# Optimization experiments

Hardware: AMD Instinct MI355X
Metric: run time of the kernel (lower is better)

The kernel has to match this reference:

```python
import jax, jax.numpy as jnp
import numpy as np

B, T, F_, H = 128, 256, 36, 128
FREQ_INV = jnp.array([1.0 / 24.0, 1.0 / 168.0, 1.0 / 720.0], dtype=jnp.float32)
WRT = 0.1


def setup_inputs() -> dict:
    key = jax.random.key(0)
    ks = jax.random.split(key, 20)

    def unif(k, shape, s):
        return jax.random.uniform(k, shape, jnp.float32, -s, s)

    sH = 1.0 / np.sqrt(H)
    sF = 1.0 / np.sqrt(F_)
    s2F = 1.0 / np.sqrt(2 * F_)

    # data layout: [B, 24, T, F]; forward direction uses channels 0..11:
    # 0 originals, 1 masks (binary), 2 deltas (nonneg), 3/6/9 remainders,
    # 4/7/10 trends, 5/8/11 seasonals.
    data = jax.random.normal(ks[0], (B, 24, T, F_), dtype=jnp.float32)
    masks = (jax.random.uniform(ks[1], (B, T, F_)) > 0.2).astype(jnp.float32)
    deltas = jax.random.uniform(ks[2], (B, T, F_)) * 5.0
    data = data.at[:, 1, :, :].set(masks)
    data = data.at[:, 2, :, :].set(deltas)

    return {
        "data": data,
        "W_dh": unif(ks[3], (H, F_), sH),   # TemporalDecay(F->H)
        "b_dh": unif(ks[4], (H,), sH),
        "W_dx": unif(ks[5], (F_, F_), sF),  # TemporalDecay diag (F->F)
        "b_dx": unif(ks[6], (F_,), sF),
        "W_hist": unif(ks[7], (F_, H), sH),  # Linear(H, F)
        "b_hist": unif(ks[8], (F_,), sH),
        "W_feat": unif(ks[9], (F_, F_), sF),
        "b_feat": unif(ks[10], (F_,), sF),
        "W_wc": unif(ks[11], (F_, 2 * F_), s2F),  # Linear(2F, F)
        "b_wc": unif(ks[12], (F_,), s2F),
        "W_ih": unif(ks[13], (4 * H, 2 * F_), sH),  # LSTMCell
        "W_hh": unif(ks[14], (4 * H, H), sH),
        "b_ih": unif(ks[15], (4 * H,), sH),
        "b_hh": unif(ks[16], (4 * H,), sH),
        "W_comb": jax.random.normal(ks[17], (1, 3), dtype=jnp.float32),  # weight_sumone_linear(3,1)
    }


def reference(data, W_dh, b_dh, W_dx, b_dx, W_hist, b_hist, W_feat, b_feat,
              W_wc, b_wc, W_ih, W_hh, b_ih, b_hh, W_comb):
    Bn, _, Tn, Fd = data.shape
    Hh = W_hh.shape[1]

    masks = data[:, 1]   # [B,T,F]
    deltas = data[:, 2]
    r = jnp.stack([data[:, 3], data[:, 6], data[:, 9]], axis=1)    # [B,3,T,F]
    tr = jnp.stack([data[:, 4], data[:, 7], data[:, 10]], axis=1)
    se = jnp.stack([data[:, 5], data[:, 8], data[:, 11]], axis=1)

    # time-major for scan
    m_T = jnp.moveaxis(masks, 1, 0)    # [T,B,F]
    d_T = jnp.moveaxis(deltas, 1, 0)
    r_T = jnp.moveaxis(r, 2, 0)        # [T,B,3,F]
    tr_T = jnp.moveaxis(tr, 2, 0)
    se_T = jnp.moveaxis(se, 2, 0)

    wk = jax.nn.softmax(W_comb, axis=1)[0]          # [3], sums to 1
    Wf_masked = W_feat * (1.0 - jnp.eye(Fd, dtype=data.dtype))
    w_dx_diag = jnp.diagonal(W_dx)                   # diag TemporalDecay
    reg_term = WRT * jnp.sum(wk * FREQ_INV)          # added every timestep

    def comb(x):  # weight_sumone_linear over the 3-decomposition axis
        return jnp.einsum('bkf,k->bf', x, wk)

    def step(carry, xs):
        h, c, loss = carry
        m2, d2, rt, trt, st = xs
        m = jnp.broadcast_to(m2[:, None, :], rt.shape)  # [B,3,F]
        d = jnp.broadcast_to(d2[:, None, :], rt.shape)

        gamma_h = jnp.exp(-jax.nn.relu(jnp.einsum('bkf,hf->bkh', d, W_dh) + b_dh))
        gamma_x = jnp.exp(-jax.nn.relu(d * w_dx_diag + b_dx))
        h = h * gamma_h

        x_h = jnp.einsum('bkh,fh->bkf', h, W_hist) + b_hist
        denom = jnp.sum(comb(m)) + 1e-5
        loss = loss + jnp.sum(comb(jnp.abs(rt - x_h) * m)) / denom

        x_c = m * rt + (1.0 - m) * x_h
        z_h = jnp.einsum('bkf,gf->bkg', x_c, Wf_masked) + b_feat
        loss = loss + jnp.sum(comb(jnp.abs(rt - z_h) * m)) / denom

        alpha = jnp.einsum('bkf,gf->bkg', jnp.concatenate([gamma_x, m], axis=2), W_wc) + b_wc
        c_h = alpha * z_h + (1.0 - alpha) * x_h
        loss = loss + jnp.sum(comb(jnp.abs(rt - c_h) * m)) / denom
        loss = loss + reg_term

        c_c = m * rt + (1.0 - m) * c_h
        inp = jnp.concatenate([c_c, m], axis=2).reshape(-1, 2 * Fd)  # [B*3, 2F]
        hf = h.reshape(-1, Hh)
        cf = c.reshape(-1, Hh)
        # PyTorch LSTMCell: gates ordered i, f, g, o. (dropout is identity in eval)
        gates = inp @ W_ih.T + b_ih + hf @ W_hh.T + b_hh
        i, f, g, o = jnp.split(gates, 4, axis=1)
        cf = jax.nn.sigmoid(f) * cf + jax.nn.sigmoid(i) * jnp.tanh(g)
        hf = jax.nn.sigmoid(o) * jnp.tanh(cf)
        h = hf.reshape(-1, 3, Hh)
        c = cf.reshape(-1, 3, Hh)

        impute = comb(c_c + st + trt)  # [B,F]
        return (h, c, loss), impute

    h0 = jnp.zeros((Bn, 3, Hh), dtype=data.dtype)
    c0 = jnp.zeros((Bn, 3, Hh), dtype=data.dtype)
    (hT, cT, loss), imput_T = jax.lax.scan(
        step, (h0, c0, jnp.float32(0.0)), (m_T, d_T, r_T, tr_T, se_T))
    imputations = jnp.moveaxis(imput_T, 0, 1)  # [B,T,F]
    return loss, imputations
```

## Files before the change

kernel.cpp:

```cpp
#include <hip/hip_runtime.h>
#include <math.h>

#define Bn 128
#define Tn 256
#define Fn 36
#define Hn 128
#define G4 512
#define BTFn (Bn*Tn*Fn)
#define TF 9216

#define INVD_OFF 0
#define LOSS_OFF 102656
#define IMP_OFF  103040

#define OFF_WHIST  0
#define OFF_WF     2304
#define OFF_WWC    2952
#define OFF_WDHT   4248
#define OFF_IN     6552
#define OFF_DP     6732
#define OFF_MP     6752
#define OFF_GXP    6792
#define OFF_XCP    6812
#define OFF_CCP    6832
#define OFF_ALPHA  6852
#define OFF_HP     6888
#define OFF_GF     6952
#define OFF_INVD   7464
#define OFF_BH     7720
#define OFF_BF     7756
#define OFF_BWC    7792
#define OFF_BDH    7828
#define OFF_WDXD   7956
#define OFF_BDX    7992
#define SMEM_WORDS 8028

typedef _Float16 h2_t __attribute__((ext_vector_type(2)));

__device__ __forceinline__ unsigned int bcu(float x) { return __builtin_bit_cast(unsigned int, x); }
__device__ __forceinline__ unsigned int pkh(float a, float b) {
    return __builtin_bit_cast(unsigned int, __builtin_amdgcn_cvt_pkrtz(a, b));
}
__device__ __forceinline__ float dot2(unsigned int a, unsigned int b, float c) {
    return __builtin_amdgcn_fdot2(__builtin_bit_cast(h2_t, a), __builtin_bit_cast(h2_t, b), c, false);
}
__device__ __forceinline__ float sigmoid_f(float x) {
    return __builtin_amdgcn_rcpf(1.f + __expf(-x));
}
__device__ __forceinline__ float tanh_f(float x) {
    return fmaf(2.f, __builtin_amdgcn_rcpf(1.f + __expf(-2.f * x)), -1.f);
}

__global__ void prep_kernel(const float* __restrict__ data,
                            float* __restrict__ ws) {
    int t = blockIdx.x;
    int tid = threadIdx.x;
    __shared__ float red[256];
    float s = 0.f;
    for (int idx = tid; idx < Bn * Fn; idx += 256) {
        int b = idx / Fn, f = idx - b * Fn;
        s += data[((size_t)(b * 24 + 1) * Tn + t) * Fn + f];
    }
    red[tid] = s;
    __syncthreads();
    for (int off = 128; off > 0; off >>= 1) {
        if (tid < off) red[tid] += red[tid + off];
        __syncthreads();
    }
    if (tid == 0) ws[INVD_OFF + t] = 1.f / (red[0] + 1e-5f);
}

#define DOT18(acc, base, woff) do {                                    \
    const unsigned int* _p = &smem[(base)];                            \
    float _a = 0.f, _b = 0.f;                                          \
    float4 _v0 = *(const float4*)_p;                                   \
    _a = dot2(bcu(_v0.x), wi[(woff) + 0], _a);                         \
    _b = dot2(bcu(_v0.y), wi[(woff) + 1], _b);                         \
    _a = dot2(bcu(_v0.z), wi[(woff) + 2], _a);                         \
    _b = dot2(bcu(_v0.w), wi[(woff) + 3], _b);                         \
    float4 _v1 = *(const float4*)(_p + 4);                             \
    _a = dot2(bcu(_v1.x), wi[(woff) + 4], _a);                         \
    _b = dot2(bcu(_v1.y), wi[(woff) + 5], _b);                         \
    _a = dot2(bcu(_v1.z), wi[(woff) + 6], _a);                         \
    _b = dot2(bcu(_v1.w), wi[(woff) + 7], _b);                         \
    float4 _v2 = *(const float4*)(_p + 8);                             \
    _a = dot2(bcu(_v2.x), wi[(woff) + 8], _a);                         \
    _b = dot2(bcu(_v2.y), wi[(woff) + 9], _b);                         \
    _a = dot2(bcu(_v2.z), wi[(woff) + 10], _a);                        \
    _b = dot2(bcu(_v2.w), wi[(woff) + 11], _b);                        \
    float4 _v3 = *(const float4*)(_p + 12);                            \
    _a = dot2(bcu(_v3.x), wi[(woff) + 12], _a);                        \
    _b = dot2(bcu(_v3.y), wi[(woff) + 13], _b);                        \
    _a = dot2(bcu(_v3.z), wi[(woff) + 14], _a);                        \
    _b = dot2(bcu(_v3.w), wi[(woff) + 15], _b);                        \
    float2 _v4 = *(const float2*)(_p + 16);                            \
    _a = dot2(bcu(_v4.x), wi[(woff) + 16], _a);                        \
    _b = dot2(bcu(_v4.y), wi[(woff) + 17], _b);                        \
    acc += _a + _b;                                                    \
} while (0)

#define STAGE(v, P) do {                                                          \
    if (lw == 0) {                                                                \
        *(float4*)&smf[OFF_IN + 4 * lu] = (v);                                    \
        smem[OFF_MP + (P) * 20 + 2 * lu]     = pkh((v).x, (v).y);                 \
        smem[OFF_MP + (P) * 20 + 2 * lu + 1] = pkh((v).z, (v).w);                 \
    } else if (lw == 1) {                                                         \
        smem[OFF_DP + 2 * lu]     = pkh((v).x, (v).y);                            \
        smem[OFF_DP + 2 * lu + 1] = pkh((v).z, (v).w);                            \
        float4 _wd = *(const float4*)&smf[OFF_WDXD + 4 * lu];                     \
        float4 _bd = *(const float4*)&smf[OFF_BDX + 4 * lu];                      \
        float _g0 = __expf(-fmaxf(fmaf((v).x, _wd.x, _bd.x), 0.f));               \
        float _g1 = __expf(-fmaxf(fmaf((v).y, _wd.y, _bd.y), 0.f));               \
        float _g2 = __expf(-fmaxf(fmaf((v).z, _wd.z, _bd.z), 0.f));               \
        float _g3 = __expf(-fmaxf(fmaf((v).w, _wd.w, _bd.w), 0.f));               \
        smem[OFF_GXP + 2 * lu]     = pkh(_g0, _g1);                               \
        smem[OFF_GXP + 2 * lu + 1] = pkh(_g2, _g3);                               \
    } else {                                                                      \
        *(float4*)&smf[OFF_IN + lw * 36 + 4 * lu] = (v);                          \
    }                                                                             \
} while (0)

__global__ __launch_bounds__(512) void rits_main(
    const float* __restrict__ data,
    const float* __restrict__ W_dh, const float* __restrict__ b_dh,
    const float* __restrict__ W_dx, const float* __restrict__ b_dx,
    const float* __restrict__ W_hist, const float* __restrict__ b_hist,
    const float* __restrict__ W_feat, const float* __restrict__ b_feat,
    const float* __restrict__ W_wc, const float* __restrict__ b_wc,
    const float* __restrict__ W_ih, const float* __restrict__ W_hh,
    const float* __restrict__ b_ih, const float* __restrict__ b_hh,
    const float* __restrict__ W_comb,
    float* __restrict__ ws) {

    extern __shared__ unsigned int smem[];
    float* smf = (float*)smem;

    const int tid = threadIdx.x;
    const int chain = blockIdx.x;
    const int b = chain / 3, k = chain - 3 * b;

    for (int i = tid; i < 64 * Fn; i += 512) {
        int q = i / Fn, f = i - q * Fn;
        float2 wv = *(const float2*)&W_hist[f * Hn + 2 * q];
        smem[OFF_WHIST + i] = pkh(wv.x, wv.y);
    }
    for (int i = tid; i < 18 * Fn; i += 512) {
        int q = i / Fn, g = i - q * Fn;
        float2 wv = *(const float2*)&W_feat[g * Fn + 2 * q];
        float w0 = (2 * q     == g) ? 0.f : wv.x;
        float w1 = (2 * q + 1 == g) ? 0.f : wv.y;
        smem[OFF_WF + i] = pkh(w0, w1);
    }
    for (int i = tid; i < 36 * Fn; i += 512) {
        int q = i / Fn, g = i - q * Fn;
        int col = (q < 18) ? 2 * q : Fn + 2 * (q - 18);
        float2 wv = *(const float2*)&W_wc[g * 2 * Fn + col];
        smem[OFF_WWC + i] = pkh(wv.x, wv.y);
    }
    for (int i = tid; i < 18 * 128; i += 512) {
        int q = i >> 7, u = i & 127;
        float2 wv = *(const float2*)&W_dh[u * Fn + 2 * q];
        smem[OFF_WDHT + i] = pkh(wv.x, wv.y);
    }
    if (tid < Fn) {
        smf[OFF_BH + tid]   = b_hist[tid];
        smf[OFF_BF + tid]   = b_feat[tid];
        smf[OFF_BWC + tid]  = b_wc[tid];
        smf[OFF_WDXD + tid] = W_dx[tid * Fn + tid];
        smf[OFF_BDX + tid]  = b_dx[tid];
    }
    if (tid < Hn) smf[OFF_BDH + tid] = b_dh[tid];
    for (int i = tid; i < Tn; i += 512) smf[OFF_INVD + i] = ws[INVD_OFF + i];
    if (tid < 64) smem[OFF_HP + tid] = 0;

    unsigned int wh[64];
    #pragma unroll
    for (int q = 0; q < 64; ++q) {
        float2 wv = *(const float2*)&W_hh[tid * Hn + 2 * q];
        wh[q] = pkh(wv.x, wv.y);
    }
    unsigned int wi[36];
    #pragma unroll
    for (int q = 0; q < 36; ++q) {
        float2 wv = *(const float2*)&W_ih[tid * 2 * Fn + 2 * q];
        wi[q] = pkh(wv.x, wv.y);
    }
    const float bias_j = b_ih[tid] + b_hh[tid];

    const float* ldsrc = nullptr; int lw = 0, lu = 0;
    if (tid >= 64 && tid < 109) {
        int idx = tid - 64;
        lw = idx / 9; lu = idx - 9 * lw;
        int row = (lw == 0) ? 1 : (lw == 1) ? 2 : (3 + 3 * k + (lw - 2));
        ldsrc = data + (size_t)(b * 24 + row) * TF + 4 * lu;
    }
    float* impp = ws + IMP_OFF + (size_t)(k * Bn + b) * TF;

    float creg = 0.f, hreg = 0.f, loss_acc = 0.f;
    __syncthreads();

    if (ldsrc) {
        float4 v0 = *(const float4*)(ldsrc);
        STAGE(v0, 0);
    }
    __syncthreads();
    if (tid >= 128 && tid < 164) {
        int f = tid - 128;
        float a0 = smf[OFF_BWC + f], a1 = 0.f;
        #pragma unroll
        for (int q = 0; q < 18; ++q) {
            a0 = dot2(smem[OFF_GXP + q], smem[OFF_WWC + q * Fn + f], a0);
            a1 = dot2(smem[OFF_MP + q],  smem[OFF_WWC + (18 + q) * Fn + f], a1);
        }
        smf[OFF_ALPHA + f] = a0 + a1;
    }
    __syncthreads();

    for (int t = 0; t < Tn; ++t) {
        const int par = t & 1, parn = par ^ 1;

        float4 nxt = {0, 0, 0, 0};
        if (ldsrc) nxt = *(const float4*)(ldsrc + (size_t)(t + 1) * Fn);

        float gacc;
        {
            float g0 = 0.f, g1 = 0.f, g2 = 0.f, g3 = 0.f;
            #pragma unroll
            for (int q = 0; q < 64; q += 4) {
                float4 hp = *(const float4*)&smem[OFF_HP + q];
                g0 = dot2(bcu(hp.x), wh[q],     g0);
                g1 = dot2(bcu(hp.y), wh[q + 1], g1);
                g2 = dot2(bcu(hp.z), wh[q + 2], g2);
                g3 = dot2(bcu(hp.w), wh[q + 3], g3);
            }
            gacc = (g0 + g1) + (g2 + g3);
        }
        if (tid < Fn) {
            float m  = smf[OFF_IN + tid];
            float rt = smf[OFF_IN + 72 + tid];
            float a0 = 0.f, a1 = 0.f, a2 = 0.f, a3 = 0.f;
            #pragma unroll
            for (int q = 0; q < 64; q += 4) {
                unsigned int h0 = smem[OFF_HP + q];
                unsigned int h1 = smem[OFF_HP + q + 1];
                unsigned int h2 = smem[OFF_HP + q + 2];
                unsigned int h3 = smem[OFF_HP + q + 3];
                a0 = dot2(h0, smem[OFF_WHIST + q * Fn + tid], a0);
                a1 = dot2(h1, smem[OFF_WHIST + (q + 1) * Fn + tid], a1);
                a2 = dot2(h2, smem[OFF_WHIST + (q + 2) * Fn + tid], a2);
                a3 = dot2(h3, smem[OFF_WHIST + (q + 3) * Fn + tid], a3);
            }
            float xh = (a0 + a1) + (a2 + a3) + smf[OFF_BH + tid];
            float xc = m * rt + (1.f - m) * xh;
            float xcn = __shfl_xor(xc, 1);
            if (!(tid & 1)) smem[OFF_XCP + (tid >> 1)] = pkh(xc, xcn);
            float z0 = 0.f, z1 = 0.f;
            #pragma unroll
            for (int q = 0; q < 18; q += 2) {
                z0 = dot2(smem[OFF_XCP + q], smem[OFF_WF + q * Fn + tid], z0);
                z1 = dot2(smem[OFF_XCP + q + 1], smem[OFF_WF + (q + 1) * Fn + tid], z1);
            }
            float zh = z0 + z1 + smf[OFF_BF + tid];
            float al = smf[OFF_ALPHA + tid];
            float chv = al * zh + (1.f - al) * xh;
            float cc = m * rt + (1.f - m) * chv;
            loss_acc = fmaf((fabsf(rt - xh) + fabsf(rt - zh) + fabsf(rt - chv)) * m,
                            smf[OFF_INVD + t], loss_acc);
            float ccn = __shfl_xor(cc, 1);
            if (!(tid & 1)) smem[OFF_CCP + (tid >> 1)] = pkh(cc, ccn);
            impp[(size_t)t * Fn + tid] = cc + smf[OFF_IN + 144 + tid] + smf[OFF_IN + 108 + tid];
        }
        __syncthreads();

        {
            float gA = gacc + bias_j;
            DOT18(gA, OFF_CCP, 0);
            DOT18(gA, OFF_MP + par * 20, 18);
            smf[OFF_GF + tid] = gA;
        }
        if (ldsrc) STAGE(nxt, parn);
        __syncthreads();

        if (tid < Hn) {
            float ig = smf[OFF_GF + tid];
            float fg = smf[OFF_GF + 128 + tid];
            float gg = smf[OFF_GF + 256 + tid];
            float og = smf[OFF_GF + 384 + tid];
            creg = sigmoid_f(fg) * creg + sigmoid_f(ig) * tanh_f(gg);
            float hn_ = sigmoid_f(og) * tanh_f(creg);
            float g0 = smf[OFF_BDH + tid], g1 = 0.f;
            #pragma unroll
            for (int q = 0; q < 18; q += 2) {
                g0 = dot2(smem[OFF_DP + q], smem[OFF_WDHT + q * 128 + tid], g0);
                g1 = dot2(smem[OFF_DP + q + 1], smem[OFF_WDHT + (q + 1) * 128 + tid], g1);
            }
            hreg = hn_ * __expf(-fmaxf(g0 + g1, 0.f));
            float hn2 = __shfl_xor(hreg, 1);
            if (!(tid & 1)) smem[OFF_HP + (tid >> 1)] = pkh(hreg, hn2);
        } else if (tid < 164) {
            int f = tid - 128;
            float a0 = smf[OFF_BWC + f], a1 = 0.f;
            #pragma unroll
            for (int q = 0; q < 18; ++q) {
                a0 = dot2(smem[OFF_GXP + q], smem[OFF_WWC + q * Fn + f], a0);
                a1 = dot2(smem[OFF_MP + parn * 20 + q], smem[OFF_WWC + (18 + q) * Fn + f], a1);
            }
            smf[OFF_ALPHA + f] = a0 + a1;
        }
        __syncthreads();
    }

    if (tid < Fn) smf[OFF_GF + tid] = loss_acc;
    __syncthreads();
    if (tid == 0) {
        float s = 0.f;
        for (int i = 0; i < Fn; ++i) s += smf[OFF_GF + i];
        float w0 = W_comb[0], w1 = W_comb[1], w2 = W_comb[2];
        float mx = fmaxf(w0, fmaxf(w1, w2));
        float e0 = expf(w0 - mx), e1 = expf(w1 - mx), e2 = expf(w2 - mx);
        float wkk = ((k == 0) ? e0 : (k == 1) ? e1 : e2) / (e0 + e1 + e2);
        ws[LOSS_OFF + chain] = s * wkk;
    }
}

__global__ void impute_reduce(const float* __restrict__ ws,
                              const float* __restrict__ W_comb,
                              float* __restrict__ out) {
    int idx = blockIdx.x * 256 + threadIdx.x;
    float w0 = W_comb[0], w1 = W_comb[1], w2 = W_comb[2];
    float mx = fmaxf(w0, fmaxf(w1, w2));
    float e0 = expf(w0 - mx), e1 = expf(w1 - mx), e2 = expf(w2 - mx);
    float inv = 1.f / (e0 + e1 + e2);
    const float* imp = ws + IMP_OFF;
    out[1 + idx] = (e0 * imp[idx] + e1 * imp[BTFn + idx] + e2 * imp[2 * BTFn + idx]) * inv;
}

__global__ void loss_final(const float* __restrict__ ws,
                           const float* __restrict__ W_comb,
                           float* __restrict__ out) {
    int tid = threadIdx.x;
    __shared__ float red[512];
    const float* lp = ws + LOSS_OFF;
    red[tid] = (tid < 384) ? lp[tid] : 0.f;
    __syncthreads();
    for (int off = 256; off > 0; off >>= 1) {
        if (tid < off) red[tid] += red[tid + off];
        __syncthreads();
    }
    if (tid == 0) {
        float w0 = W_comb[0], w1 = W_comb[1], w2 = W_comb[2];
        float mx = fmaxf(w0, fmaxf(w1, w2));
        float e0 = expf(w0 - mx), e1 = expf(w1 - mx), e2 = expf(w2 - mx);
        float inv = 1.f / (e0 + e1 + e2);
        float wk0 = e0 * inv, wk1 = e1 * inv, wk2 = e2 * inv;
        float reg = 0.1f * (wk0 * (1.f / 24.f) + wk1 * (1.f / 168.f) + wk2 * (1.f / 720.f));
        out[0] = red[0] + (float)Tn * reg;
    }
}

extern "C" void kernel_launch(void* const* d_in, const int* in_sizes, int n_in,
                              void* d_out, int out_size, void* d_ws, size_t ws_size,
                              hipStream_t stream) {
    const float* data   = (const float*)d_in[0];
    const float* W_dh   = (const float*)d_in[1];
    const float* b_dh   = (const float*)d_in[2];
    const float* W_dx   = (const float*)d_in[3];
    const float* b_dx   = (const float*)d_in[4];
    const float* W_hist = (const float*)d_in[5];
    const float* b_hist = (const float*)d_in[6];
    const float* W_feat = (const float*)d_in[7];
    const float* b_feat = (const float*)d_in[8];
    const float* W_wc   = (const float*)d_in[9];
    const float* b_wc   = (const float*)d_in[10];
    const float* W_ih   = (const float*)d_in[11];
    const float* W_hh   = (const float*)d_in[12];
    const float* b_ih   = (const float*)d_in[13];
    const float* b_hh   = (const float*)d_in[14];
    const float* W_comb = (const float*)d_in[15];
    float* ws = (float*)d_ws;
    float* out = (float*)d_out;

    hipLaunchKernelGGL(prep_kernel, dim3(Tn), dim3(256), 0, stream, data, ws);
    hipLaunchKernelGGL(rits_main, dim3(Bn * 3), dim3(512), SMEM_WORDS * 4, stream,
                       data, W_dh, b_dh, W_dx, b_dx, W_hist, b_hist,
                       W_feat, b_feat, W_wc, b_wc, W_ih, W_hh, b_ih, b_hh, W_comb, ws);
    hipLaunchKernelGGL(impute_reduce, dim3(BTFn / 256), dim3(256), 0, stream, ws, W_comb, out);
    hipLaunchKernelGGL(loss_final, dim3(1), dim3(512), 0, stream, ws, W_comb, out);
}
```

Measured before the change: 1.146 ms.

## Prefetch inputs four steps ahead, hoist mask gate dot, batch imputation stores

Unrolls the time loop by four and loads each loader thread's inputs four timesteps ahead into registers, using twice as many loader threads with float2 loads in place of float4. Global-load latency then sits further off the serial recurrence. The mask half of the input-gate dot product is computed in the previous phase, off the critical path between barriers. Imputation stores are buffered and written once per four steps. The cost is more registers in a kernel that already holds large weight arrays in registers, so occupancy or spilling may suffer.

```diff
diff --git a/kernel.cpp b/kernel.cpp
--- a/kernel.cpp
+++ b/kernel.cpp
@@ -101,22 +101,17 @@
 
 #define STAGE(v, P) do {                                                          \
     if (lw == 0) {                                                                \
-        *(float4*)&smf[OFF_IN + 4 * lu] = (v);                                    \
-        smem[OFF_MP + (P) * 20 + 2 * lu]     = pkh((v).x, (v).y);                 \
-        smem[OFF_MP + (P) * 20 + 2 * lu + 1] = pkh((v).z, (v).w);                 \
+        *(float2*)&smf[OFF_IN + 2 * lu] = (v);                                    \
+        smem[OFF_MP + (P) * 20 + lu] = pkh((v).x, (v).y);                         \
     } else if (lw == 1) {                                                         \
-        smem[OFF_DP + 2 * lu]     = pkh((v).x, (v).y);                            \
-        smem[OFF_DP + 2 * lu + 1] = pkh((v).z, (v).w);                            \
-        float4 _wd = *(const float4*)&smf[OFF_WDXD + 4 * lu];                     \
-        float4 _bd = *(const float4*)&smf[OFF_BDX + 4 * lu];                      \
+        smem[OFF_DP + lu] = pkh((v).x, (v).y);                                    \
+        float2 _wd = *(const float2*)&smf[OFF_WDXD + 2 * lu];                     \
+        float2 _bd = *(const float2*)&smf[OFF_BDX + 2 * lu];                      \
         float _g0 = __expf(-fmaxf(fmaf((v).x, _wd.x, _bd.x), 0.f));               \
         float _g1 = __expf(-fmaxf(fmaf((v).y, _wd.y, _bd.y), 0.f));               \
-        float _g2 = __expf(-fmaxf(fmaf((v).z, _wd.z, _bd.z), 0.f));               \
-        float _g3 = __expf(-fmaxf(fmaf((v).w, _wd.w, _bd.w), 0.f));               \
-        smem[OFF_GXP + 2 * lu]     = pkh(_g0, _g1);                               \
-        smem[OFF_GXP + 2 * lu + 1] = pkh(_g2, _g3);                               \
+        smem[OFF_GXP + lu] = pkh(_g0, _g1);                                       \
     } else {                                                                      \
-        *(float4*)&smf[OFF_IN + lw * 36 + 4 * lu] = (v);                          \
+        *(float2*)&smf[OFF_IN + lw * 36 + 2 * lu] = (v);                          \
     }                                                                             \
 } while (0)
 
@@ -188,20 +183,25 @@
     const float bias_j = b_ih[tid] + b_hh[tid];
 
     const float* ldsrc = nullptr; int lw = 0, lu = 0;
-    if (tid >= 64 && tid < 109) {
+    if (tid >= 64 && tid < 154) {
         int idx = tid - 64;
-        lw = idx / 9; lu = idx - 9 * lw;
+        lw = idx / 18; lu = idx - 18 * lw;
         int row = (lw == 0) ? 1 : (lw == 1) ? 2 : (3 + 3 * k + (lw - 2));
-        ldsrc = data + (size_t)(b * 24 + row) * TF + 4 * lu;
+        ldsrc = data + (size_t)(b * 24 + row) * TF + 2 * lu;
     }
     float* impp = ws + IMP_OFF + (size_t)(k * Bn + b) * TF;
 
-    float creg = 0.f, hreg = 0.f, loss_acc = 0.f;
-    __syncthreads();
-
+    float creg = 0.f, hreg = 0.f, loss_acc = 0.f, gm = 0.f;
+    __syncthreads();
+
+    float2 cur1 = {0,0}, cur2 = {0,0}, cur3 = {0,0};
+    float2 nxt0 = {0,0}, nxt1 = {0,0}, nxt2 = {0,0}, nxt3 = {0,0};
     if (ldsrc) {
-        float4 v0 = *(const float4*)(ldsrc);
-        STAGE(v0, 0);
+        float2 c0 = *(const float2*)(ldsrc);
+        cur1 = *(const float2*)(ldsrc + Fn);
+        cur2 = *(const float2*)(ldsrc + 2 * Fn);
+        cur3 = *(const float2*)(ldsrc + 3 * Fn);
+        STAGE(c0, 0);
     }
     __syncthreads();
     if (tid >= 128 && tid < 164) {
@@ -214,100 +214,125 @@
         }
         smf[OFF_ALPHA + f] = a0 + a1;
     }
-    __syncthreads();
-
-    for (int t = 0; t < Tn; ++t) {
-        const int par = t & 1, parn = par ^ 1;
-
-        float4 nxt = {0, 0, 0, 0};
-        if (ldsrc) nxt = *(const float4*)(ldsrc + (size_t)(t + 1) * Fn);
-
-        float gacc;
-        {
-            float g0 = 0.f, g1 = 0.f, g2 = 0.f, g3 = 0.f;
-            #pragma unroll
-            for (int q = 0; q < 64; q += 4) {
-                float4 hp = *(const float4*)&smem[OFF_HP + q];
-                g0 = dot2(bcu(hp.x), wh[q],     g0);
-                g1 = dot2(bcu(hp.y), wh[q + 1], g1);
-                g2 = dot2(bcu(hp.z), wh[q + 2], g2);
-                g3 = dot2(bcu(hp.w), wh[q + 3], g3);
-            }
-            gacc = (g0 + g1) + (g2 + g3);
+    DOT18(gm, OFF_MP, 18);
+    __syncthreads();
+
+    for (int t8 = 0; t8 < Tn; t8 += 4) {
+        float iv0 = 0.f, iv1 = 0.f, iv2 = 0.f, iv3 = 0.f;
+        #pragma unroll
+        for (int s = 0; s < 4; ++s) {
+            const int t = t8 + s;
+            const int par = s & 1, parn = par ^ 1;
+
+            if (s == 0 && ldsrc) {
+                nxt0 = *(const float2*)(ldsrc + (size_t)(t8 + 4) * Fn);
+                nxt1 = *(const float2*)(ldsrc + (size_t)(t8 + 5) * Fn);
+                nxt2 = *(const float2*)(ldsrc + (size_t)(t8 + 6) * Fn);
+                nxt3 = *(const float2*)(ldsrc + (size_t)(t8 + 7) * Fn);
+            }
+            float gacc;
+            {
+                float g0 = 0.f, g1 = 0.f, g2 = 0.f, g3 = 0.f;
+                #pragma unroll
+                for (int q = 0; q < 64; q += 4) {
+                    float4 hp = *(const float4*)&smem[OFF_HP + q];
+                    g0 = dot2(bcu(hp.x), wh[q],     g0);
+                    g1 = dot2(bcu(hp.y), wh[q + 1], g1);
+                    g2 = dot2(bcu(hp.z), wh[q + 2], g2);
+                    g3 = dot2(bcu(hp.w), wh[q + 3], g3);
+                }
+                gacc = (g0 + g1) + (g2 + g3);
+            }
+            if (tid < Fn) {
+                float m  = smf[OFF_IN + tid];
+                float rt = smf[OFF_IN + 72 + tid];
+                float a0 = 0.f, a1 = 0.f, a2 = 0.f, a3 = 0.f;
+                #pragma unroll
+                for (int q = 0; q < 64; q += 4) {
+                    unsigned int h0 = smem[OFF_HP + q];
+                    unsigned int h1 = smem[OFF_HP + q + 1];
+                    unsigned int h2 = smem[OFF_HP + q + 2];
+                    unsigned int h3 = smem[OFF_HP + q + 3];
+                    a0 = dot2(h0, smem[OFF_WHIST + q * Fn + tid], a0);
+                    a1 = dot2(h1, smem[OFF_WHIST + (q + 1) * Fn + tid], a1);
+                    a2 = dot2(h2, smem[OFF_WHIST + (q + 2) * Fn + tid], a2);
+                    a3 = dot2(h3, smem[OFF_WHIST + (q + 3) * Fn + tid], a3);
+                }
+                float xh = (a0 + a1) + (a2 + a3) + smf[OFF_BH + tid];
+                float xc = m * rt + (1.f - m) * xh;
+                float xcn = __shfl_xor(xc, 1);
+                if (!(tid & 1)) smem[OFF_XCP + (tid >> 1)] = pkh(xc, xcn);
+                float z0 = 0.f, z1 = 0.f;
+                #pragma unroll
+                for (int q = 0; q < 18; q += 2) {
+                    z0 = dot2(smem[OFF_XCP + q], smem[OFF_WF + q * Fn + tid], z0);
+                    z1 = dot2(smem[OFF_XCP + q + 1], smem[OFF_WF + (q + 1) * Fn + tid], z1);
+                }
+                float zh = z0 + z1 + smf[OFF_BF + tid];
+                float al = smf[OFF_ALPHA + tid];
+                float chv = al * zh + (1.f - al) * xh;
+                float cc = m * rt + (1.f - m) * chv;
+                loss_acc = fmaf((fabsf(rt - xh) + fabsf(rt - zh) + fabsf(rt - chv)) * m,
+                                smf[OFF_INVD + t], loss_acc);
+                float ccn = __shfl_xor(cc, 1);
+                if (!(tid & 1)) smem[OFF_CCP + (tid >> 1)] = pkh(cc, ccn);
+                float iv = cc + smf[OFF_IN + 144 + tid] + smf[OFF_IN + 108 + tid];
+                if (s == 0) iv0 = iv; else if (s == 1) iv1 = iv;
+                else if (s == 2) iv2 = iv; else iv3 = iv;
+            }
+            __syncthreads();
+
+            {
+                float gA = gacc + gm + bias_j;
+                DOT18(gA, OFF_CCP, 0);
+                smf[OFF_GF + tid] = gA;
+            }
+            if (ldsrc) {
+                if (s == 0) STAGE(cur1, parn);
+                else if (s == 1) STAGE(cur2, parn);
+                else if (s == 2) STAGE(cur3, parn);
+                else STAGE(nxt0, parn);
+            }
+            __syncthreads();
+
+            if (tid < Hn) {
+                float ig = smf[OFF_GF + tid];
+                float fg = smf[OFF_GF + 128 + tid];
+                float gg = smf[OFF_GF + 256 + tid];
+                float og = smf[OFF_GF + 384 + tid];
+                creg = sigmoid_f(fg) * creg + sigmoid_f(ig) * tanh_f(gg);
+                float hn_ = sigmoid_f(og) * tanh_f(creg);
+                float g0 = smf[OFF_BDH + tid], g1 = 0.f;
+                #pragma unroll
+                for (int q = 0; q < 18; q += 2) {
+                    g0 = dot2(smem[OFF_DP + q], smem[OFF_WDHT + q * 128 + tid], g0);
+                    g1 = dot2(smem[OFF_DP + q + 1], smem[OFF_WDHT + (q + 1) * 128 + tid], g1);
+                }
+                hreg = hn_ * __expf(-fmaxf(g0 + g1, 0.f));
+                float hn2 = __shfl_xor(hreg, 1);
+                if (!(tid & 1)) smem[OFF_HP + (tid >> 1)] = pkh(hreg, hn2);
+            } else if (tid < 164) {
+                int f = tid - 128;
+                float a0 = smf[OFF_BWC + f], a1 = 0.f;
+                #pragma unroll
+                for (int q = 0; q < 18; ++q) {
+                    a0 = dot2(smem[OFF_GXP + q], smem[OFF_WWC + q * Fn + f], a0);
+                    a1 = dot2(smem[OFF_MP + parn * 20 + q], smem[OFF_WWC + (18 + q) * Fn + f], a1);
+                }
+                smf[OFF_ALPHA + f] = a0 + a1;
+            }
+            gm = 0.f;
+            DOT18(gm, OFF_MP + parn * 20, 18);
+            __syncthreads();
+
+            if (s == 3 && tid < Fn) {
+                impp[(size_t)t8 * Fn + tid]       = iv0;
+                impp[(size_t)(t8 + 1) * Fn + tid] = iv1;
+                impp[(size_t)(t8 + 2) * Fn + tid] = iv2;
+                impp[(size_t)(t8 + 3) * Fn + tid] = iv3;
+            }
         }
-        if (tid < Fn) {
-            float m  = smf[OFF_IN + tid];
-            float rt = smf[OFF_IN + 72 + tid];
-            float a0 = 0.f, a1 = 0.f, a2 = 0.f, a3 = 0.f;
-            #pragma unroll
-            for (int q = 0; q < 64; q += 4) {
-                unsigned int h0 = smem[OFF_HP + q];
-                unsigned int h1 = smem[OFF_HP + q + 1];
-                unsigned int h2 = smem[OFF_HP + q + 2];
-                unsigned int h3 = smem[OFF_HP + q + 3];
-                a0 = dot2(h0, smem[OFF_WHIST + q * Fn + tid], a0);
-                a1 = dot2(h1, smem[OFF_WHIST + (q + 1) * Fn + tid], a1);
-                a2 = dot2(h2, smem[OFF_WHIST + (q + 2) * Fn + tid], a2);
-                a3 = dot2(h3, smem[OFF_WHIST + (q + 3) * Fn + tid], a3);
-            }
-            float xh = (a0 + a1) + (a2 + a3) + smf[OFF_BH + tid];
-            float xc = m * rt + (1.f - m) * xh;
-            float xcn = __shfl_xor(xc, 1);
-            if (!(tid & 1)) smem[OFF_XCP + (tid >> 1)] = pkh(xc, xcn);
-            float z0 = 0.f, z1 = 0.f;
-            #pragma unroll
-            for (int q = 0; q < 18; q += 2) {
-                z0 = dot2(smem[OFF_XCP + q], smem[OFF_WF + q * Fn + tid], z0);
-                z1 = dot2(smem[OFF_XCP + q + 1], smem[OFF_WF + (q + 1) * Fn + tid], z1);
-            }
-            float zh = z0 + z1 + smf[OFF_BF + tid];
-            float al = smf[OFF_ALPHA + tid];
-            float chv = al * zh + (1.f - al) * xh;
-            float cc = m * rt + (1.f - m) * chv;
-            loss_acc = fmaf((fabsf(rt - xh) + fabsf(rt - zh) + fabsf(rt - chv)) * m,
-                            smf[OFF_INVD + t], loss_acc);
-            float ccn = __shfl_xor(cc, 1);
-            if (!(tid & 1)) smem[OFF_CCP + (tid >> 1)] = pkh(cc, ccn);
-            impp[(size_t)t * Fn + tid] = cc + smf[OFF_IN + 144 + tid] + smf[OFF_IN + 108 + tid];
-        }
-        __syncthreads();
-
-        {
-            float gA = gacc + bias_j;
-            DOT18(gA, OFF_CCP, 0);
-            DOT18(gA, OFF_MP + par * 20, 18);
-            smf[OFF_GF + tid] = gA;
-        }
-        if (ldsrc) STAGE(nxt, parn);
-        __syncthreads();
-
-        if (tid < Hn) {
-            float ig = smf[OFF_GF + tid];
-            float fg = smf[OFF_GF + 128 + tid];
-            float gg = smf[OFF_GF + 256 + tid];
-            float og = smf[OFF_GF + 384 + tid];
-            creg = sigmoid_f(fg) * creg + sigmoid_f(ig) * tanh_f(gg);
-            float hn_ = sigmoid_f(og) * tanh_f(creg);
-            float g0 = smf[OFF_BDH + tid], g1 = 0.f;
-            #pragma unroll
-            for (int q = 0; q < 18; q += 2) {
-                g0 = dot2(smem[OFF_DP + q], smem[OFF_WDHT + q * 128 + tid], g0);
-                g1 = dot2(smem[OFF_DP + q + 1], smem[OFF_WDHT + (q + 1) * 128 + tid], g1);
-            }
-            hreg = hn_ * __expf(-fmaxf(g0 + g1, 0.f));
-            float hn2 = __shfl_xor(hreg, 1);
-            if (!(tid & 1)) smem[OFF_HP + (tid >> 1)] = pkh(hreg, hn2);
-        } else if (tid < 164) {
-            int f = tid - 128;
-            float a0 = smf[OFF_BWC + f], a1 = 0.f;
-            #pragma unroll
-            for (int q = 0; q < 18; ++q) {
-                a0 = dot2(smem[OFF_GXP + q], smem[OFF_WWC + q * Fn + f], a0);
-                a1 = dot2(smem[OFF_MP + parn * 20 + q], smem[OFF_WWC + (18 + q) * Fn + f], a1);
-            }
-            smf[OFF_ALPHA + f] = a0 + a1;
-        }
-        __syncthreads();
+        if (ldsrc) { cur1 = nxt1; cur2 = nxt2; cur3 = nxt3; }
     }
 
     if (tid < Fn) smf[OFF_GF + tid] = loss_acc;
```

Result: faster. 1.016 ms (median of 2 runs) (-11.4%).
